# Optimization experiments

Hardware: AMD Instinct MI355X
Metric: run time of the kernel (lower is better)

Reference implementation:

```python
import jax, jax.numpy as jnp
import numpy as np

N, NS, IN_P, OUT_P, SHARE = 65536, 16, 256, 256, 8
MID = OUT_P
EPS = 1e-5


def _bn(x, gamma, beta):
    # torch BatchNorm1d (training mode, biased var) applied over the channel
    # (last) axis; stats over all other axes. Matches BN on x.transpose(1,2).
    mean = x.mean(axis=(0, 1), keepdims=True)
    var = ((x - mean) ** 2).mean(axis=(0, 1), keepdims=True)
    return gamma * (x - mean) * jax.lax.rsqrt(var + EPS) + beta


def setup_inputs() -> dict:
    key = jax.random.key(0)
    ks = jax.random.split(key, 12)
    w = lambda k, shape: jax.random.normal(k, shape, dtype=jnp.float32) * 0.02
    return {
        "p": jax.random.uniform(ks[0], (N, 3), dtype=jnp.float32),
        "x": jax.random.normal(ks[1], (N, IN_P), dtype=jnp.float32),
        "idx": jax.random.randint(ks[2], (N, NS), 0, N),
        "wq": w(ks[3], (MID, IN_P)), "bq": jnp.zeros((MID,), jnp.float32),
        "wk": w(ks[4], (MID, IN_P)), "bk": jnp.zeros((MID,), jnp.float32),
        "wv": w(ks[5], (OUT_P, IN_P)), "bv": jnp.zeros((OUT_P,), jnp.float32),
        "wp1": w(ks[6], (3, 3)), "bp1": jnp.zeros((3,), jnp.float32),
        "gp": jnp.ones((3,), jnp.float32), "btp": jnp.zeros((3,), jnp.float32),
        "wp2": w(ks[7], (OUT_P, 3)), "bp2": jnp.zeros((OUT_P,), jnp.float32),
        "g1": jnp.ones((MID,), jnp.float32), "b1": jnp.zeros((MID,), jnp.float32),
        "ww1": w(ks[8], (MID // SHARE, MID)), "bw1": jnp.zeros((MID // SHARE,), jnp.float32),
        "g2": jnp.ones((MID // SHARE,), jnp.float32), "b2": jnp.zeros((MID // SHARE,), jnp.float32),
        "ww2": w(ks[9], (OUT_P // SHARE, OUT_P // SHARE)), "bw2": jnp.zeros((OUT_P // SHARE,), jnp.float32),
    }


def reference(p, x, idx, wq, bq, wk, bk, wv, bv, wp1, bp1, gp, btp, wp2, bp2,
              g1, b1, ww1, bw1, g2, b2, ww2, bw2):
    # q/k/v projections: [N, C]
    xq = x @ wq.T + bq
    xk = x @ wk.T + bk
    xv = x @ wv.T + bv
    # queryandgroup: gather neighbor features + relative positions
    xk_g = xk[idx]                      # [N, NS, MID]
    xv_g = xv[idx]                      # [N, NS, OUT_P]
    p_r = p[idx] - p[:, None, :]        # [N, NS, 3]  (use_xyz relative coords)
    # linear_p: Linear(3,3) -> BN(3) -> ReLU -> Linear(3, OUT_P)
    p_r = p_r @ wp1.T + bp1
    p_r = jax.nn.relu(_bn(p_r, gp, btp))
    p_r = p_r @ wp2.T + bp2             # [N, NS, OUT_P]
    # vector attention logits; out_planes // mid_planes == 1 so the
    # view(...).sum(2) of p_r is just p_r
    w = xk_g - xq[:, None, :] + p_r     # [N, NS, MID]
    # linear_w: BN -> ReLU -> Linear(MID, MID/S) -> BN -> ReLU -> Linear
    w = jax.nn.relu(_bn(w, g1, b1))
    w = w @ ww1.T + bw1                 # [N, NS, MID/S]
    w = jax.nn.relu(_bn(w, g2, b2))
    w = w @ ww2.T + bw2                 # [N, NS, OUT_P/S]
    w = jax.nn.softmax(w, axis=1)       # softmax over neighbors
    # grouped weighted sum with shared attention planes
    n, ns, c = xv_g.shape
    out = ((xv_g + p_r).reshape(n, ns, SHARE, c // SHARE)
           * w[:, :, None, :]).sum(axis=1).reshape(n, c)
    return out
```

## Files before the change

### kernel.cpp

```cpp
#include <hip/hip_runtime.h>
#include <hip/hip_bf16.h>

#define NPTS 65536
#define NSAMP 16
#define CH 256
#define CNT (NPTS * NSAMP)
#define EPSV 1e-5f

typedef __hip_bfloat16 bf16;
typedef __attribute__((ext_vector_type(8))) short short8;
typedef __attribute__((ext_vector_type(4))) short sh4;
typedef __attribute__((ext_vector_type(4))) float floatx4;

__device__ __forceinline__ float b2f(bf16 v) { return __bfloat162float(v); }

__device__ __forceinline__ float s2f(short v) {
    return __uint_as_float(((unsigned)(unsigned short)v) << 16);
}

__device__ __forceinline__ short f2bf_bits(float f) {
    bf16 h = __float2bfloat16(f);
    short s;
    __builtin_memcpy(&s, &h, 2);
    return s;
}

__global__ __launch_bounds__(256) void fused0_kernel(
    const float* __restrict__ wq, const float* __restrict__ wk,
    const float* __restrict__ wv, const float* __restrict__ ww2,
    const float* __restrict__ x, const float* __restrict__ p,
    const int* __restrict__ idx,
    const float* __restrict__ wp1, const float* __restrict__ bp1,
    bf16* __restrict__ Wcat, bf16* __restrict__ ww2b, bf16* __restrict__ xb,
    float* __restrict__ statsP, float4* __restrict__ v4)
{
    __shared__ float red[4][6];
    int bid = blockIdx.x;

    if (bid < 1024) {
        float W00 = wp1[0], W01 = wp1[1], W02 = wp1[2];
        float W10 = wp1[3], W11 = wp1[4], W12 = wp1[5];
        float W20 = wp1[6], W21 = wp1[7], W22 = wp1[8];
        float B0 = bp1[0], B1 = bp1[1], B2 = bp1[2];

        float s0 = 0, s1 = 0, s2 = 0, q0 = 0, q1 = 0, q2 = 0;
        for (int r = bid * 256 + threadIdx.x; r < CNT; r += 1024 * 256) {
            int n = r >> 4;
            int i = idx[r];
            float a0 = p[3 * (size_t)i]     - p[3 * (size_t)n];
            float a1 = p[3 * (size_t)i + 1] - p[3 * (size_t)n + 1];
            float a2 = p[3 * (size_t)i + 2] - p[3 * (size_t)n + 2];
            float v0 = W00 * a0 + W01 * a1 + W02 * a2 + B0;
            float v1 = W10 * a0 + W11 * a1 + W12 * a2 + B1;
            float v2 = W20 * a0 + W21 * a1 + W22 * a2 + B2;
            s0 += v0; q0 += v0 * v0;
            s1 += v1; q1 += v1 * v1;
            s2 += v2; q2 += v2 * v2;
            v4[r] = make_float4(v0, v1, v2, 0.f);
        }
        float v[6] = {s0, s1, s2, q0, q1, q2};
        int wave = threadIdx.x >> 6;
#pragma unroll
        for (int k = 0; k < 6; k++) {
            float xv = v[k];
#pragma unroll
            for (int off = 32; off > 0; off >>= 1) xv += __shfl_down(xv, off);
            if ((threadIdx.x & 63) == 0) red[wave][k] = xv;
        }
        __syncthreads();
        if (threadIdx.x < 6) {
            float s = red[0][threadIdx.x] + red[1][threadIdx.x]
                    + red[2][threadIdx.x] + red[3][threadIdx.x];
            atomicAdd(&statsP[threadIdx.x * 16], s);
        }
    } else if (bid < 1120) {
        int e = ((bid - 1024) * 256 + threadIdx.x) * 8;
        const float* src = (e < 65536) ? wq : (e < 131072) ? wk : wv;
        int off = e & 65535;
        float4 f0 = *(const float4*)(src + off);
        float4 f1 = *(const float4*)(src + off + 4);
        short8 r;
        r[0] = f2bf_bits(f0.x); r[1] = f2bf_bits(f0.y);
        r[2] = f2bf_bits(f0.z); r[3] = f2bf_bits(f0.w);
        r[4] = f2bf_bits(f1.x); r[5] = f2bf_bits(f1.y);
        r[6] = f2bf_bits(f1.z); r[7] = f2bf_bits(f1.w);
        *(short8*)(Wcat + e) = r;
    } else if (bid == 1120) {
        int e = threadIdx.x * 4;
        float4 f = *(const float4*)(ww2 + e);
        sh4 r;
        r[0] = f2bf_bits(f.x); r[1] = f2bf_bits(f.y);
        r[2] = f2bf_bits(f.z); r[3] = f2bf_bits(f.w);
        *(sh4*)(ww2b + e) = r;
    } else {
        size_t e = ((size_t)(bid - 1121) * 256 + threadIdx.x) * 8;
        float4 f0 = *(const float4*)(x + e);
        float4 f1 = *(const float4*)(x + e + 4);
        short8 r;
        r[0] = f2bf_bits(f0.x); r[1] = f2bf_bits(f0.y);
        r[2] = f2bf_bits(f0.z); r[3] = f2bf_bits(f0.w);
        r[4] = f2bf_bits(f1.x); r[5] = f2bf_bits(f1.y);
        r[6] = f2bf_bits(f1.z); r[7] = f2bf_bits(f1.w);
        *(short8*)(xb + e) = r;
    }
}

__global__ __launch_bounds__(256) void gemm_kernel(
    const bf16* __restrict__ xb, const bf16* __restrict__ Wcat,
    const float* __restrict__ bq, const float* __restrict__ bk,
    const float* __restrict__ bv,
    bf16* __restrict__ xq, bf16* __restrict__ xk, bf16* __restrict__ xv)
{
    __shared__ __align__(16) bf16 As[128 * 40];
    __shared__ __align__(16) bf16 Bs[128 * 40];

    int t = threadIdx.x, lane = t & 63, wave = t >> 6;
    int m0 = blockIdx.x * 128;
    int y = blockIdx.y, n0 = y * 128;
    int srow = t >> 1, sch = t & 1;
    int m = lane & 15, q = lane >> 4;
    int wm = wave >> 1, wn = wave & 1;

    floatx4 acc[4][4];
#pragma unroll
    for (int a = 0; a < 4; a++)
#pragma unroll
        for (int b = 0; b < 4; b++) acc[a][b] = (floatx4){0.f, 0.f, 0.f, 0.f};

    for (int kk = 0; kk < 256; kk += 32) {
        const bf16* ap = xb + (size_t)(m0 + srow) * 256 + kk + sch * 16;
        *(short8*)&As[srow * 40 + sch * 16]     = *(const short8*)ap;
        *(short8*)&As[srow * 40 + sch * 16 + 8] = *(const short8*)(ap + 8);
        const bf16* bp = Wcat + (size_t)(n0 + srow) * 256 + kk + sch * 16;
        *(short8*)&Bs[srow * 40 + sch * 16]     = *(const short8*)bp;
        *(short8*)&Bs[srow * 40 + sch * 16 + 8] = *(const short8*)(bp + 8);
        __syncthreads();

        short8 av[4], bvv[4];
#pragma unroll
        for (int mt = 0; mt < 4; mt++)
            av[mt] = *(const short8*)&As[(wm * 64 + mt * 16 + m) * 40 + q * 8];
#pragma unroll
        for (int nt = 0; nt < 4; nt++)
            bvv[nt] = *(const short8*)&Bs[(wn * 64 + nt * 16 + m) * 40 + q * 8];
#pragma unroll
        for (int mt = 0; mt < 4; mt++)
#pragma unroll
            for (int nt = 0; nt < 4; nt++)
                acc[mt][nt] = __builtin_amdgcn_mfma_f32_16x16x32_bf16(av[mt], bvv[nt], acc[mt][nt], 0, 0, 0);
        __syncthreads();
    }

    int z = y >> 1;
    bf16* O        = (z == 0) ? xq : (z == 1) ? xk : xv;
    const float* B = (z == 0) ? bq : (z == 1) ? bk : bv;
    int cbase = (y & 1) * 128 + wn * 64;
#pragma unroll
    for (int nt = 0; nt < 4; nt++) {
        int oc = cbase + nt * 16 + m;
        float bias = B[oc];
#pragma unroll
        for (int mt = 0; mt < 4; mt++) {
            int grow = m0 + wm * 64 + mt * 16 + q * 4;
#pragma unroll
            for (int i = 0; i < 4; i++)
                O[(size_t)(grow + i) * 256 + oc] = __float2bfloat16(acc[mt][nt][i] + bias);
        }
    }
}

__global__ void finalize_kernel(const float* __restrict__ stats,
                                const float* __restrict__ gamma,
                                const float* __restrict__ beta,
                                float* __restrict__ ss, int nch, int sstr)
{
    int c = threadIdx.x;
    if (c < nch) {
        float inv = 1.0f / (float)CNT;
        float mean = stats[c * sstr] * inv;
        float var = stats[(nch + c) * sstr] * inv - mean * mean;
        float sc = gamma[c] * rsqrtf(var + EPSV);
        ss[c] = sc;
        ss[nch + c] = beta[c] - mean * sc;
    }
}

__global__ __launch_bounds__(256) void stats1_kernel(
    const int* __restrict__ idx, const float4* __restrict__ r4,
    const bf16* __restrict__ xk, const bf16* __restrict__ xq,
    const float* __restrict__ wp2, const float* __restrict__ bp2,
    const float* __restrict__ ssP, float* __restrict__ stats1)
{
    __shared__ int idxs[1024];
    __shared__ float redS[8 * 264];
    __shared__ float redQ[8 * 264];

    int t = threadIdx.x;
    int r0 = blockIdx.x * 1024;
    for (int e = t; e < 1024; e += 256) idxs[e] = idx[r0 + e];

    int sub = t & 31, rl = t >> 5, cb = sub * 8;
    float w0[8], w1[8], w2[8], bc[8];
#pragma unroll
    for (int k = 0; k < 8; k++) {
        w0[k] = wp2[3 * (cb + k)];
        w1[k] = wp2[3 * (cb + k) + 1];
        w2[k] = wp2[3 * (cb + k) + 2];
        bc[k] = bp2[cb + k];
    }
    float scP0 = ssP[0], scP1 = ssP[1], scP2 = ssP[2];
    float shP0 = ssP[3], shP1 = ssP[4], shP2 = ssP[5];
    float s8[8] = {0, 0, 0, 0, 0, 0, 0, 0};
    float q8[8] = {0, 0, 0, 0, 0, 0, 0, 0};
    __syncthreads();

#pragma unroll 4
    for (int rr = rl; rr < 1024; rr += 8) {
        int r = r0 + rr;
        int i = idxs[rr];
        float4 va = r4[r];
        float rx = fmaxf(scP0 * va.x + shP0, 0.f);
        float ry = fmaxf(scP1 * va.y + shP1, 0.f);
        float rz = fmaxf(scP2 * va.z + shP2, 0.f);
        short8 kv = *(const short8*)(xk + (size_t)i * 256 + cb);
        short8 qv = *(const short8*)(xq + (size_t)(r >> 4) * 256 + cb);
#pragma unroll
        for (int k = 0; k < 8; k++) {
            float w = s2f(kv[k]) - s2f(qv[k]) + rx * w0[k] + ry * w1[k] + rz * w2[k] + bc[k];
            s8[k] += w; q8[k] += w * w;
        }
    }
#pragma unroll
    for (int k = 0; k < 8; k++) {
        redS[rl * 264 + cb + k] = s8[k];
        redQ[rl * 264 + cb + k] = q8[k];
    }
    __syncthreads();
    int c = t;
    float ts = 0, tq = 0;
#pragma unroll
    for (int sr = 0; sr < 8; sr++) {
        ts += redS[sr * 264 + c];
        tq += redQ[sr * 264 + c];
    }
    atomicAdd(&stats1[c], ts);
    atomicAdd(&stats1[256 + c], tq);
}

__global__ __launch_bounds__(512, 4) void stats2_kernel(
    const int* __restrict__ idx, const float4* __restrict__ r4,
    const bf16* __restrict__ xk, const bf16* __restrict__ xq,
    const float* __restrict__ wp2, const float* __restrict__ bp2,
    const float* __restrict__ ssP, const float* __restrict__ ss1,
    const float* __restrict__ ww1, const float* __restrict__ bw1,
    bf16* __restrict__ y2, float* __restrict__ stats2)
{
    __shared__ __align__(16) bf16 hb0[64 * 256];
    __shared__ __align__(16) bf16 hb1[64 * 256];

    int t = threadIdx.x;
    int lane = t & 63, wave = t >> 6;
    int m = lane & 15, q = lane >> 4;
    int wr = wave >> 1, wc = wave & 1;
    int sub = t & 31, rl = t >> 5, cb = sub * 8;
    int r0 = blockIdx.x * 1024;

    short8 bf[8];
#pragma unroll
    for (int k = 0; k < 8; k++) {
        const float* wp = ww1 + (wc * 16 + m) * 256 + k * 32 + q * 8;
        float4 u0 = *(const float4*)(wp);
        float4 u1 = *(const float4*)(wp + 4);
        short8 b;
        b[0] = f2bf_bits(u0.x); b[1] = f2bf_bits(u0.y);
        b[2] = f2bf_bits(u0.z); b[3] = f2bf_bits(u0.w);
        b[4] = f2bf_bits(u1.x); b[5] = f2bf_bits(u1.y);
        b[6] = f2bf_bits(u1.z); b[7] = f2bf_bits(u1.w);
        bf[k] = b;
    }

    float w0[8], w1[8], w2[8], bc[8], s1c[8], t1c[8];
#pragma unroll
    for (int k = 0; k < 8; k++) {
        w0[k] = wp2[3 * (cb + k)];
        w1[k] = wp2[3 * (cb + k) + 1];
        w2[k] = wp2[3 * (cb + k) + 2];
        bc[k] = bp2[cb + k];
        s1c[k] = ss1[cb + k];
        t1c[k] = ss1[256 + cb + k];
    }
    float scP0 = ssP[0], scP1 = ssP[1], scP2 = ssP[2];
    float shP0 = ssP[3], shP1 = ssP[4], shP2 = ssP[5];
    float bwv = bw1[wc * 16 + m];
    float jsum = 0, jsq = 0;
    int swh = cb ^ ((rl & 7) << 3);
    int swa = (m & 7) << 3;

#pragma unroll
    for (int u = 0; u < 4; u++) {
        int rr = rl + u * 16;
        int r = r0 + rr;
        int i = idx[r];
        float4 va = r4[r];
        float rx = fmaxf(scP0 * va.x + shP0, 0.f);
        float ry = fmaxf(scP1 * va.y + shP1, 0.f);
        float rz = fmaxf(scP2 * va.z + shP2, 0.f);
        short8 kv = *(const short8*)(xk + (size_t)i * 256 + cb);
        short8 qv = *(const short8*)(xq + (size_t)(r >> 4) * 256 + cb);
        short8 h;
#pragma unroll
        for (int k = 0; k < 8; k++) {
            float w = s2f(kv[k]) - s2f(qv[k]) + rx * w0[k] + ry * w1[k] + rz * w2[k] + bc[k];
            h[k] = f2bf_bits(fmaxf(s1c[k] * w + t1c[k], 0.f));
        }
        *(short8*)&hb0[rr * 256 + swh] = h;
    }

    for (int it = 0; it < 16; ++it) {
        __syncthreads();

        int rbn = r0 + (it + 1) * 64;
        bf16* hbw = (it & 1) ? hb0 : hb1;
        const bf16* abase = ((it & 1) ? hb1 : hb0) + (wr * 16 + m) * 256;

        short8 kvs[4];
        if (it < 15) {
#pragma unroll
            for (int u = 0; u < 4; u++) {
                int r = rbn + rl + u * 16;
                kvs[u] = *(const short8*)(xk + (size_t)idx[r] * 256 + cb);
            }
        }

        floatx4 a = (floatx4){bwv, bwv, bwv, bwv};
#pragma unroll
        for (int k = 0; k < 8; k++) {
            int col = (k * 32 + q * 8) ^ swa;
            short8 af = *(const short8*)(abase + col);
            a = __builtin_amdgcn_mfma_f32_16x16x32_bf16(af, bf[k], a, 0, 0, 0);
        }
        int grow = r0 + it * 64 + wr * 16 + q * 4;
#pragma unroll
        for (int ii = 0; ii < 4; ii++) {
            float y = a[ii];
            jsum += y; jsq += y * y;
            y2[(size_t)(grow + ii) * 32 + wc * 16 + m] = __float2bfloat16(y);
        }

        if (it < 15) {
#pragma unroll
            for (int u = 0; u < 4; u++) {
                int rr = rl + u * 16;
                int r = rbn + rr;
                float4 va = r4[r];
                float rx = fmaxf(scP0 * va.x + shP0, 0.f);
                float ry = fmaxf(scP1 * va.y + shP1, 0.f);
                float rz = fmaxf(scP2 * va.z + shP2, 0.f);
                short8 qv = *(const short8*)(xq + (size_t)(r >> 4) * 256 + cb);
                short8 h;
#pragma unroll
                for (int k = 0; k < 8; k++) {
                    float w = s2f(kvs[u][k]) - s2f(qv[k]) + rx * w0[k] + ry * w1[k] + rz * w2[k] + bc[k];
                    h[k] = f2bf_bits(fmaxf(s1c[k] * w + t1c[k], 0.f));
                }
                *(short8*)&hbw[rr * 256 + swh] = h;
            }
        }
    }

    jsum += __shfl_xor(jsum, 16); jsum += __shfl_xor(jsum, 32);
    jsq  += __shfl_xor(jsq, 16);  jsq  += __shfl_xor(jsq, 32);
    if (q == 0) {
        atomicAdd(&stats2[wc * 16 + m], jsum);
        atomicAdd(&stats2[32 + wc * 16 + m], jsq);
    }
}

__global__ __launch_bounds__(256) void final_kernel(
    const int* __restrict__ idx, const float4* __restrict__ r4,
    const bf16* __restrict__ xv,
    const float* __restrict__ wp2, const float* __restrict__ bp2,
    const bf16* __restrict__ y2, const float* __restrict__ ss2,
    const bf16* __restrict__ ww2b, const float* __restrict__ bw2,
    const float* __restrict__ ssP, float* __restrict__ out)
{
    __shared__ __align__(16) float wsm[4][16][36];
    __shared__ float Asm[4][4][32];

    int t = threadIdx.x, wave = t >> 6, lane = t & 63;
    int m = lane & 15, q = lane >> 4;

    short8 bf0 = *(const short8*)(ww2b + m * 32 + q * 8);
    short8 bf1 = *(const short8*)(ww2b + (16 + m) * 32 + q * 8);
    float bwj0 = bw2[m], bwj1 = bw2[16 + m];

    float s2c[8], t2c[8];
#pragma unroll
    for (int k = 0; k < 8; k++) {
        s2c[k] = ss2[q * 8 + k];
        t2c[k] = ss2[32 + q * 8 + k];
    }
    float scP0 = ssP[0], scP1 = ssP[1], scP2 = ssP[2];
    float shP0 = ssP[3], shP1 = ssP[4], shP2 = ssP[5];

    int c0 = lane * 4;
    int j4 = (lane & 7) * 4;
    float wpc0[4], wpc1[4], wpc2[4], bpc[4];
#pragma unroll
    for (int k = 0; k < 4; k++) {
        wpc0[k] = wp2[(c0 + k) * 3];
        wpc1[k] = wp2[(c0 + k) * 3 + 1];
        wpc2[k] = wp2[(c0 + k) * 3 + 2];
        bpc[k]  = bp2[c0 + k];
    }

    int pbase = (blockIdx.x * 4 + wave) * 8;
    for (int pp = 0; pp < 8; pp++) {
        int n = pbase + pp;
        size_t rbase = (size_t)n * 16;

        int iv = idx[rbase + m];

        short8 yv = *(const short8*)(y2 + (rbase + m) * 32 + q * 8);
        short8 av;
#pragma unroll
        for (int k = 0; k < 8; k++)
            av[k] = f2bf_bits(fmaxf(s2c[k] * s2f(yv[k]) + t2c[k], 0.f));

        floatx4 l0 = (floatx4){bwj0, bwj0, bwj0, bwj0};
        floatx4 l1 = (floatx4){bwj1, bwj1, bwj1, bwj1};
        l0 = __builtin_amdgcn_mfma_f32_16x16x32_bf16(av, bf0, l0, 0, 0, 0);
        l1 = __builtin_amdgcn_mfma_f32_16x16x32_bf16(av, bf1, l1, 0, 0, 0);

        float mx0 = fmaxf(fmaxf(l0[0], l0[1]), fmaxf(l0[2], l0[3]));
        float mx1 = fmaxf(fmaxf(l1[0], l1[1]), fmaxf(l1[2], l1[3]));
        mx0 = fmaxf(mx0, __shfl_xor(mx0, 16));
        mx0 = fmaxf(mx0, __shfl_xor(mx0, 32));
        mx1 = fmaxf(mx1, __shfl_xor(mx1, 16));
        mx1 = fmaxf(mx1, __shfl_xor(mx1, 32));
        float w0[4], w1[4];
        float sum0 = 0.f, sum1 = 0.f;
#pragma unroll
        for (int i = 0; i < 4; i++) {
            w0[i] = __expf(l0[i] - mx0); sum0 += w0[i];
            w1[i] = __expf(l1[i] - mx1); sum1 += w1[i];
        }
        sum0 += __shfl_xor(sum0, 16); sum0 += __shfl_xor(sum0, 32);
        sum1 += __shfl_xor(sum1, 16); sum1 += __shfl_xor(sum1, 32);
        float inv0 = 1.f / sum0, inv1 = 1.f / sum1;

        float A00 = 0, A10 = 0, A20 = 0, A30 = 0;
        float A01 = 0, A11 = 0, A21 = 0, A31 = 0;
#pragma unroll
        for (int i = 0; i < 4; i++) {
            w0[i] *= inv0; w1[i] *= inv1;
            float4 va = r4[rbase + q * 4 + i];
            float rx = fmaxf(scP0 * va.x + shP0, 0.f);
            float ry = fmaxf(scP1 * va.y + shP1, 0.f);
            float rz = fmaxf(scP2 * va.z + shP2, 0.f);
            A00 += rx * w0[i]; A10 += ry * w0[i];
            A20 += rz * w0[i]; A30 += w0[i];
            A01 += rx * w1[i]; A11 += ry * w1[i];
            A21 += rz * w1[i]; A31 += w1[i];
            wsm[wave][q * 4 + i][m]      = w0[i];
            wsm[wave][q * 4 + i][16 + m] = w1[i];
        }
        A00 += __shfl_xor(A00, 16); A00 += __shfl_xor(A00, 32);
        A10 += __shfl_xor(A10, 16); A10 += __shfl_xor(A10, 32);
        A20 += __shfl_xor(A20, 16); A20 += __shfl_xor(A20, 32);
        A30 += __shfl_xor(A30, 16); A30 += __shfl_xor(A30, 32);
        A01 += __shfl_xor(A01, 16); A01 += __shfl_xor(A01, 32);
        A11 += __shfl_xor(A11, 16); A11 += __shfl_xor(A11, 32);
        A21 += __shfl_xor(A21, 16); A21 += __shfl_xor(A21, 32);
        A31 += __shfl_xor(A31, 16); A31 += __shfl_xor(A31, 32);
        if (q == 0) {
            Asm[wave][0][m] = A00; Asm[wave][1][m] = A10;
            Asm[wave][2][m] = A20; Asm[wave][3][m] = A30;
            Asm[wave][0][16 + m] = A01; Asm[wave][1][16 + m] = A11;
            Asm[wave][2][16 + m] = A21; Asm[wave][3][16 + m] = A31;
        }

        float acc0 = 0, acc1 = 0, acc2 = 0, acc3 = 0;
#pragma unroll
        for (int s = 0; s < 16; s++) {
            int i = __builtin_amdgcn_readlane(iv, s);
            sh4 vv = *(const sh4*)(xv + (size_t)i * 256 + c0);
            float4 wv = *(const float4*)&wsm[wave][s][j4];
            acc0 += s2f(vv[0]) * wv.x;
            acc1 += s2f(vv[1]) * wv.y;
            acc2 += s2f(vv[2]) * wv.z;
            acc3 += s2f(vv[3]) * wv.w;
        }

        float res[4] = {acc0, acc1, acc2, acc3};
#pragma unroll
        for (int k = 0; k < 4; k++) {
            int j = j4 + k;
            res[k] += wpc0[k] * Asm[wave][0][j] + wpc1[k] * Asm[wave][1][j]
                    + wpc2[k] * Asm[wave][2][j] + bpc[k]  * Asm[wave][3][j];
        }
        *(float4*)(out + (size_t)n * 256 + c0) =
            make_float4(res[0], res[1], res[2], res[3]);
    }
}

extern "C" void kernel_launch(void* const* d_in, const int* in_sizes, int n_in,
                              void* d_out, int out_size, void* d_ws, size_t ws_size,
                              hipStream_t stream) {
    (void)in_sizes; (void)n_in; (void)out_size; (void)ws_size;

    const float* p   = (const float*)d_in[0];
    const float* x   = (const float*)d_in[1];
    const int*   idx = (const int*)d_in[2];
    const float* wq  = (const float*)d_in[3];  const float* bq  = (const float*)d_in[4];
    const float* wk  = (const float*)d_in[5];  const float* bk  = (const float*)d_in[6];
    const float* wv  = (const float*)d_in[7];  const float* bv  = (const float*)d_in[8];
    const float* wp1 = (const float*)d_in[9];  const float* bp1 = (const float*)d_in[10];
    const float* gp  = (const float*)d_in[11]; const float* btp = (const float*)d_in[12];
    const float* wp2 = (const float*)d_in[13]; const float* bp2 = (const float*)d_in[14];
    const float* g1  = (const float*)d_in[15]; const float* b1  = (const float*)d_in[16];
    const float* ww1 = (const float*)d_in[17]; const float* bw1 = (const float*)d_in[18];
    const float* g2  = (const float*)d_in[19]; const float* b2  = (const float*)d_in[20];
    const float* ww2 = (const float*)d_in[21]; const float* bw2 = (const float*)d_in[22];
    float* out = (float*)d_out;

    float* fws    = (float*)d_ws;
    float* statsP = fws;
    float* ssP    = fws + 96;
    float* stats1 = fws + 112;
    float* ss1    = fws + 624;
    float* stats2 = fws + 1136;
    float* ss2    = fws + 1200;
    bf16* ww2b = (bf16*)((char*)d_ws + 6144);
    bf16* Wcat = (bf16*)((char*)d_ws + 8192);
    bf16* xq = (bf16*)((char*)d_ws + 401408);
    bf16* xk = xq + (size_t)NPTS * CH;
    bf16* xv = xk + (size_t)NPTS * CH;
    bf16* y2 = xv + (size_t)NPTS * CH;
    float4* r4 = (float4*)(y2 + (size_t)CNT * 32);
    bf16* xb = y2;

    hipMemsetAsync(d_ws, 0, 8192, stream);

    fused0_kernel<<<1024 + 97 + 8192, 256, 0, stream>>>(
        wq, wk, wv, ww2, x, p, idx, wp1, bp1, Wcat, ww2b, xb, statsP, r4);
    gemm_kernel<<<dim3(512, 6), 256, 0, stream>>>(xb, Wcat, bq, bk, bv, xq, xk, xv);
    finalize_kernel<<<1, 256, 0, stream>>>(statsP, gp, btp, ssP, 3, 16);
    stats1_kernel<<<1024, 256, 0, stream>>>(idx, r4, xk, xq, wp2, bp2, ssP, stats1);
    finalize_kernel<<<1, 256, 0, stream>>>(stats1, g1, b1, ss1, 256, 1);
    stats2_kernel<<<1024, 512, 0, stream>>>(idx, r4, xk, xq, wp2, bp2, ssP, ss1, ww1, bw1, y2, stats2);
    finalize_kernel<<<1, 256, 0, stream>>>(stats2, g2, b2, ss2, 32, 1);
    final_kernel<<<NPTS / 32, 256, 0, stream>>>(idx, r4, xv, wp2, bp2, y2, ss2, ww2b, bw2, ssP, out);
}
```

Before: 775.5 us.

## Halve stats2 block size so each wave computes both 16-column MFMA tiles

The stats2 kernel now runs 256 threads per block instead of 512. Each wave now computes both 16-column output halves of the 256->32 projection, reusing each LDS A-fragment load for two MFMAs. Each thread also builds 8 gathered rows per 64-row tile instead of 4, and the y2 output stores become nontemporal. The aim is to cut redundant LDS A-fragment reads and the separate per-wave-column split, at the cost of more registers per thread and fewer threads per block to hide gather latency.

```diff
diff --git a/kernel.cpp b/kernel.cpp
--- a/kernel.cpp
+++ b/kernel.cpp
@@ -247,7 +247,7 @@
     atomicAdd(&stats1[256 + c], tq);
 }
 
-__global__ __launch_bounds__(512, 4) void stats2_kernel(
+__global__ __launch_bounds__(256) void stats2_kernel(
     const int* __restrict__ idx, const float4* __restrict__ r4,
     const bf16* __restrict__ xk, const bf16* __restrict__ xq,
     const float* __restrict__ wp2, const float* __restrict__ bp2,
@@ -261,22 +261,28 @@
     int t = threadIdx.x;
     int lane = t & 63, wave = t >> 6;
     int m = lane & 15, q = lane >> 4;
-    int wr = wave >> 1, wc = wave & 1;
     int sub = t & 31, rl = t >> 5, cb = sub * 8;
     int r0 = blockIdx.x * 1024;
 
-    short8 bf[8];
+    short8 bf0[8], bf1[8];
 #pragma unroll
     for (int k = 0; k < 8; k++) {
-        const float* wp = ww1 + (wc * 16 + m) * 256 + k * 32 + q * 8;
-        float4 u0 = *(const float4*)(wp);
-        float4 u1 = *(const float4*)(wp + 4);
-        short8 b;
-        b[0] = f2bf_bits(u0.x); b[1] = f2bf_bits(u0.y);
-        b[2] = f2bf_bits(u0.z); b[3] = f2bf_bits(u0.w);
-        b[4] = f2bf_bits(u1.x); b[5] = f2bf_bits(u1.y);
-        b[6] = f2bf_bits(u1.z); b[7] = f2bf_bits(u1.w);
-        bf[k] = b;
+        const float* w0p = ww1 + m * 256 + k * 32 + q * 8;
+        const float* w1p = ww1 + (16 + m) * 256 + k * 32 + q * 8;
+        float4 u0 = *(const float4*)(w0p);
+        float4 u1 = *(const float4*)(w0p + 4);
+        float4 u2 = *(const float4*)(w1p);
+        float4 u3 = *(const float4*)(w1p + 4);
+        short8 b0, b1;
+        b0[0] = f2bf_bits(u0.x); b0[1] = f2bf_bits(u0.y);
+        b0[2] = f2bf_bits(u0.z); b0[3] = f2bf_bits(u0.w);
+        b0[4] = f2bf_bits(u1.x); b0[5] = f2bf_bits(u1.y);
+        b0[6] = f2bf_bits(u1.z); b0[7] = f2bf_bits(u1.w);
+        b1[0] = f2bf_bits(u2.x); b1[1] = f2bf_bits(u2.y);
+        b1[2] = f2bf_bits(u2.z); b1[3] = f2bf_bits(u2.w);
+        b1[4] = f2bf_bits(u3.x); b1[5] = f2bf_bits(u3.y);
+        b1[6] = f2bf_bits(u3.z); b1[7] = f2bf_bits(u3.w);
+        bf0[k] = b0; bf1[k] = b1;
     }
 
     float w0[8], w1[8], w2[8], bc[8], s1c[8], t1c[8];
@@ -291,29 +297,31 @@
     }
     float scP0 = ssP[0], scP1 = ssP[1], scP2 = ssP[2];
     float shP0 = ssP[3], shP1 = ssP[4], shP2 = ssP[5];
-    float bwv = bw1[wc * 16 + m];
-    float jsum = 0, jsq = 0;
-    int swh = cb ^ ((rl & 7) << 3);
+    float bw0 = bw1[m], bw16 = bw1[16 + m];
+    float jsum0 = 0, jsum1 = 0, jsq0 = 0, jsq1 = 0;
+    int swh = cb ^ (rl << 3);
     int swa = (m & 7) << 3;
 
-#pragma unroll
-    for (int u = 0; u < 4; u++) {
-        int rr = rl + u * 16;
-        int r = r0 + rr;
-        int i = idx[r];
-        float4 va = r4[r];
-        float rx = fmaxf(scP0 * va.x + shP0, 0.f);
-        float ry = fmaxf(scP1 * va.y + shP1, 0.f);
-        float rz = fmaxf(scP2 * va.z + shP2, 0.f);
-        short8 kv = *(const short8*)(xk + (size_t)i * 256 + cb);
-        short8 qv = *(const short8*)(xq + (size_t)(r >> 4) * 256 + cb);
-        short8 h;
-#pragma unroll
-        for (int k = 0; k < 8; k++) {
-            float w = s2f(kv[k]) - s2f(qv[k]) + rx * w0[k] + ry * w1[k] + rz * w2[k] + bc[k];
-            h[k] = f2bf_bits(fmaxf(s1c[k] * w + t1c[k], 0.f));
-        }
-        *(short8*)&hb0[rr * 256 + swh] = h;
+    {
+#pragma unroll
+        for (int u = 0; u < 8; u++) {
+            int rr = rl + u * 8;
+            int r = r0 + rr;
+            int i = idx[r];
+            float4 va = r4[r];
+            float rx = fmaxf(scP0 * va.x + shP0, 0.f);
+            float ry = fmaxf(scP1 * va.y + shP1, 0.f);
+            float rz = fmaxf(scP2 * va.z + shP2, 0.f);
+            short8 kv = *(const short8*)(xk + (size_t)i * 256 + cb);
+            short8 qv = *(const short8*)(xq + (size_t)(r >> 4) * 256 + cb);
+            short8 h;
+#pragma unroll
+            for (int k = 0; k < 8; k++) {
+                float w = s2f(kv[k]) - s2f(qv[k]) + rx * w0[k] + ry * w1[k] + rz * w2[k] + bc[k];
+                h[k] = f2bf_bits(fmaxf(s1c[k] * w + t1c[k], 0.f));
+            }
+            *(short8*)&hb0[rr * 256 + swh] = h;
+        }
     }
 
     for (int it = 0; it < 16; ++it) {
@@ -321,36 +329,43 @@
 
         int rbn = r0 + (it + 1) * 64;
         bf16* hbw = (it & 1) ? hb0 : hb1;
-        const bf16* abase = ((it & 1) ? hb1 : hb0) + (wr * 16 + m) * 256;
-
-        short8 kvs[4];
+        const bf16* abase = ((it & 1) ? hb1 : hb0) + (wave * 16 + m) * 256;
+
+        short8 kvs[8];
         if (it < 15) {
 #pragma unroll
-            for (int u = 0; u < 4; u++) {
-                int r = rbn + rl + u * 16;
+            for (int u = 0; u < 8; u++) {
+                int r = rbn + rl + u * 8;
                 kvs[u] = *(const short8*)(xk + (size_t)idx[r] * 256 + cb);
             }
         }
 
-        floatx4 a = (floatx4){bwv, bwv, bwv, bwv};
+        floatx4 a0 = (floatx4){bw0, bw0, bw0, bw0};
+        floatx4 a1 = (floatx4){bw16, bw16, bw16, bw16};
 #pragma unroll
         for (int k = 0; k < 8; k++) {
             int col = (k * 32 + q * 8) ^ swa;
             short8 af = *(const short8*)(abase + col);
-            a = __builtin_amdgcn_mfma_f32_16x16x32_bf16(af, bf[k], a, 0, 0, 0);
-        }
-        int grow = r0 + it * 64 + wr * 16 + q * 4;
+            a0 = __builtin_amdgcn_mfma_f32_16x16x32_bf16(af, bf0[k], a0, 0, 0, 0);
+            a1 = __builtin_amdgcn_mfma_f32_16x16x32_bf16(af, bf1[k], a1, 0, 0, 0);
+        }
+        int grow = r0 + it * 64 + wave * 16 + q * 4;
 #pragma unroll
         for (int ii = 0; ii < 4; ii++) {
-            float y = a[ii];
-            jsum += y; jsq += y * y;
-            y2[(size_t)(grow + ii) * 32 + wc * 16 + m] = __float2bfloat16(y);
+            float y0 = a0[ii];
+            float y1 = a1[ii];
+            jsum0 += y0; jsq0 += y0 * y0;
+            jsum1 += y1; jsq1 += y1 * y1;
+            __builtin_nontemporal_store(f2bf_bits(y0),
+                (short*)(y2 + (size_t)(grow + ii) * 32 + m));
+            __builtin_nontemporal_store(f2bf_bits(y1),
+                (short*)(y2 + (size_t)(grow + ii) * 32 + 16 + m));
         }
 
         if (it < 15) {
 #pragma unroll
-            for (int u = 0; u < 4; u++) {
-                int rr = rl + u * 16;
+            for (int u = 0; u < 8; u++) {
+                int rr = rl + u * 8;
                 int r = rbn + rr;
                 float4 va = r4[r];
                 float rx = fmaxf(scP0 * va.x + shP0, 0.f);
@@ -368,11 +383,15 @@
         }
     }
 
-    jsum += __shfl_xor(jsum, 16); jsum += __shfl_xor(jsum, 32);
-    jsq  += __shfl_xor(jsq, 16);  jsq  += __shfl_xor(jsq, 32);
+    jsum0 += __shfl_xor(jsum0, 16); jsum0 += __shfl_xor(jsum0, 32);
+    jsum1 += __shfl_xor(jsum1, 16); jsum1 += __shfl_xor(jsum1, 32);
+    jsq0  += __shfl_xor(jsq0, 16);  jsq0  += __shfl_xor(jsq0, 32);
+    jsq1  += __shfl_xor(jsq1, 16);  jsq1  += __shfl_xor(jsq1, 32);
     if (q == 0) {
-        atomicAdd(&stats2[wc * 16 + m], jsum);
-        atomicAdd(&stats2[32 + wc * 16 + m], jsq);
+        atomicAdd(&stats2[m], jsum0);
+        atomicAdd(&stats2[16 + m], jsum1);
+        atomicAdd(&stats2[32 + m], jsq0);
+        atomicAdd(&stats2[48 + m], jsq1);
     }
 }
 
@@ -548,7 +567,7 @@
     finalize_kernel<<<1, 256, 0, stream>>>(statsP, gp, btp, ssP, 3, 16);
     stats1_kernel<<<1024, 256, 0, stream>>>(idx, r4, xk, xq, wp2, bp2, ssP, stats1);
     finalize_kernel<<<1, 256, 0, stream>>>(stats1, g1, b1, ss1, 256, 1);
-    stats2_kernel<<<1024, 512, 0, stream>>>(idx, r4, xk, xq, wp2, bp2, ssP, ss1, ww1, bw1, y2, stats2);
+    stats2_kernel<<<1024, 256, 0, stream>>>(idx, r4, xk, xq, wp2, bp2, ssP, ss1, ww1, bw1, y2, stats2);
     finalize_kernel<<<1, 256, 0, stream>>>(stats2, g2, b2, ss2, 32, 1);
     final_kernel<<<NPTS / 32, 256, 0, stream>>>(idx, r4, xv, wp2, bp2, y2, ss2, ww2b, bw2, ssP, out);
 }
```

After: 643.0 us. 17.1% less time.
